# Optimization experiments

Measured on AMD Instinct MI355X. Metric: run time of the kernel, lower is better.

## Reference

```python
import jax, jax.numpy as jnp
import numpy as np

N_NODE = 4095
D_EMB = 32
D_MODEL = 64
NHEADS = 8
ALPHA = 1.0
B = N_NODE + 1  # batch must equal n_node+1 (see einsum 'nm,tmd->tnd')
T = 32


def setup_inputs() -> dict:
    key = jax.random.key(0)
    ks = jax.random.split(key, 16)
    f32 = jnp.float32
    inp = {
        "q": jax.random.normal(ks[0], (B, T, D_MODEL), f32),
        "k": jax.random.normal(ks[1], (B, T, D_MODEL), f32),
        "v": jax.random.normal(ks[2], (B, T, D_MODEL), f32),
        # learned parameters (torch init is randn; scaled for numeric stability)
        "emb": jax.random.normal(ks[3], (N_NODE + 1, D_EMB), f32) * 0.05,
        "We": jax.random.normal(ks[4], (D_EMB, D_MODEL, D_MODEL), f32) * 0.05,
        "be": jax.random.normal(ks[5], (D_EMB, D_MODEL), f32) * 0.05,
        "Wq": jax.random.normal(ks[6], (D_MODEL, D_MODEL), f32) * 0.05,
        "bq": jax.random.normal(ks[7], (D_MODEL,), f32) * 0.05,
        "Wk": jax.random.normal(ks[8], (D_MODEL, D_MODEL), f32) * 0.05,
        "bk": jax.random.normal(ks[9], (D_MODEL,), f32) * 0.05,
        "Wv": jax.random.normal(ks[10], (D_MODEL, D_MODEL), f32) * 0.05,
        "bv": jax.random.normal(ks[11], (D_MODEL,), f32) * 0.05,
        "Wo": jax.random.normal(ks[12], (D_MODEL, D_MODEL), f32) * 0.05,
        "bo": jax.random.normal(ks[13], (D_MODEL,), f32) * 0.05,
    }
    return inp


def _elu(x, alpha):
    return jnp.where(x > 0, x, alpha * (jnp.exp(x) - 1.0))


def _split_heads(x, h):
    # torch.cat(torch.split(x, D//h, dim=-1), dim=0): [B,T,D] -> [h*B,T,D/h]
    b, t, d = x.shape
    return jnp.moveaxis(x.reshape(b, t, h, d // h), 2, 0).reshape(h * b, t, d // h)


def _merge_heads(x, b, h):
    # torch.cat(torch.split(x, B, dim=0), dim=-1): [h*B,T,D/h] -> [B,T,D]
    hb, t, dh = x.shape
    return jnp.moveaxis(x.reshape(h, b, t, dh), 0, 2).reshape(b, t, h * dh)


def reference(q, k, v, emb, We, be, Wq, bq, Wk, bk, Wv, bv, Wo, bo):
    Bq, Tq, D = q.shape
    h = NHEADS
    scale = (D // h) ** 0.5

    # linear projections (torch Linear: x @ W.T + b)
    q = q @ Wq.T + bq
    k = k @ Wk.T + bk
    v = v @ Wv.T + bv

    # adjacency: sum over d_emb of pairwise diff == s_i - s_j (same math, no [N,N,E] tensor)
    s = jnp.sum(emb, axis=-1)  # [N+1]
    sim = s[:, None] - s[None, :]  # [N+1, N+1]
    A = jax.nn.softmax(_elu(sim, ALPHA), axis=-1) + jnp.eye(Bq, dtype=q.dtype)

    # updateQ: adjacency-weighted diffusion + per-node weight matrices
    qt = jnp.transpose(q, (1, 0, 2))  # [T, N, D]
    W = jnp.einsum('ne,eio->nio', emb, We)  # [N, D, D]
    b = emb @ be  # [N, D]
    q_ = jnp.einsum('nm,tmd->tnd', A, qt)  # diffusion
    q_ = jnp.einsum('tnd,ndo->tno', q_, W) + b  # per-node matmul
    q = jnp.transpose(q_, (1, 0, 2))  # [N, T, D]

    # manual multi-head attention via split/cat
    qh = _split_heads(q, h)
    kh = _split_heads(k, h)
    vh = _split_heads(v, h)
    attn = jax.nn.softmax(jnp.einsum('btd,bsd->bts', qh, kh) / scale, axis=-1)
    out = jnp.einsum('bts,bsd->btd', attn, vh)
    out = _merge_heads(out, Bq, h)
    return out @ Wo.T + bo
```

## Files before the change

kernel.cpp:

```cpp
#include <hip/hip_runtime.h>
#include <hip/hip_bf16.h>

constexpr int NN  = 4096;
constexpr int DE  = 32;
constexpr int TD  = 2048;

typedef __attribute__((ext_vector_type(8))) short short8;
typedef __attribute__((ext_vector_type(4))) float f32x4;

#define MFMA16(a, b, c) __builtin_amdgcn_mfma_f32_16x16x32_bf16(a, b, c, 0, 0, 0)

__device__ inline ushort f2b(float x) {
    __hip_bfloat16 h = __float2bfloat16(x);
    union { __hip_bfloat16 h; ushort u; } c; c.h = h;
    return c.u;
}

__device__ inline float b2f(ushort u) {
    union { unsigned u; float f; } c; c.u = ((unsigned)u) << 16;
    return c.f;
}

__device__ inline short8 pack8(float4 a, float4 b) {
    short8 v;
    v[0] = (short)f2b(a.x); v[1] = (short)f2b(a.y); v[2] = (short)f2b(a.z); v[3] = (short)f2b(a.w);
    v[4] = (short)f2b(b.x); v[5] = (short)f2b(b.y); v[6] = (short)f2b(b.z); v[7] = (short)f2b(b.w);
    return v;
}

__device__ inline short8 pack8v(f32x4 a, f32x4 b) {
    short8 v;
    v[0] = (short)f2b(a[0]); v[1] = (short)f2b(a[1]); v[2] = (short)f2b(a[2]); v[3] = (short)f2b(a[3]);
    v[4] = (short)f2b(b[0]); v[5] = (short)f2b(b[1]); v[6] = (short)f2b(b[2]); v[7] = (short)f2b(b[3]);
    return v;
}

__device__ __forceinline__ short8 as_s8(f32x4 v) {
    union { f32x4 f; short8 s; } u; u.f = v; return u.s;
}

template<int OFF>
__device__ __forceinline__ f32x4 gl16(unsigned long long addr) {
    f32x4 d;
    asm volatile("global_load_dwordx4 %0, %1, off offset:%c2"
                 : "=v"(d) : "v"(addr), "n"(OFF) : "memory");
    return d;
}

__global__ __launch_bounds__(256) void k_prep(const float* __restrict__ emb,
                                              const float* __restrict__ We,
                                              const float* __restrict__ be,
                                              const float* __restrict__ Wk,
                                              const float* __restrict__ Wv,
                                              const float* __restrict__ Wo,
                                              float* __restrict__ s_g,
                                              ushort* __restrict__ embbf,
                                              ushort* __restrict__ WeTT,
                                              ushort* __restrict__ Wkbf,
                                              ushort* __restrict__ Wvbf,
                                              ushort* __restrict__ Wobf,
                                              float* __restrict__ bn) {
    int id = blockIdx.x, tid = threadIdx.x;
    if (id < 16) {
        int n = id * 256 + tid;
        const float4* e4 = (const float4*)(emb + n * DE);
        float s = 0.f;
#pragma unroll
        for (int i = 0; i < DE / 4; ++i) { float4 v = e4[i]; s += v.x + v.y + v.z + v.w; }
        s_g[n] = s;
    } else if (id < 144) {
        int g4 = (id - 16) * 256 + tid;
        float4 v = *(const float4*)&emb[(size_t)g4 * 4];
        ushort4 o; o.x = f2b(v.x); o.y = f2b(v.y); o.z = f2b(v.z); o.w = f2b(v.w);
        *(ushort4*)&embbf[(size_t)g4 * 4] = o;
    } else if (id < 656) {
        int gid = (id - 144) * 256 + tid;
        int od = gid >> 5, e = gid & 31;
        int o = od >> 6, d = od & 63;
        WeTT[gid] = f2b(We[(size_t)e * 4096 + d * 64 + o]);
    } else if (id < 704) {
        int id5 = id - 656;
        int which = id5 >> 4, gid = (id5 & 15) * 256 + tid;
        const float* src = which == 0 ? Wk : (which == 1 ? Wv : Wo);
        ushort* dst = which == 0 ? Wkbf : (which == 1 ? Wvbf : Wobf);
        dst[gid] = f2b(src[gid]);
    } else {
        int gid = (id - 704) * 256 + tid;
        int n = gid >> 6, o = gid & 63;
        float acc = 0.f;
#pragma unroll
        for (int e = 0; e < DE; ++e) acc += emb[n * DE + e] * be[e * 64 + o];
        bn[gid] = acc;
    }
}

__global__ __launch_bounds__(256) void k_pr(const float* __restrict__ X,
                                            const float* __restrict__ W,
                                            const float* __restrict__ bias,
                                            ushort* __restrict__ Y,
                                            const float* __restrict__ s_g,
                                            int* __restrict__ perm) {
    __shared__ float ss[NN];
    int id = blockIdx.x, tid = threadIdx.x;
    if (id < 512) {
        int lane = tid & 63, wid = tid >> 6;
        int r0 = id * 256 + wid * 64;
        int l15 = lane & 15, kb = lane >> 4;
        f32x4 acc[4][4] = {};
#pragma unroll
        for (int kk = 0; kk < 2; ++kk) {
            short8 af[4], bf[4];
#pragma unroll
            for (int f = 0; f < 4; ++f) {
                const float* ap = X + (size_t)(r0 + f * 16 + l15) * 64 + kk * 32 + kb * 8;
                af[f] = pack8(*(const float4*)ap, *(const float4*)(ap + 4));
                const float* bp = W + (size_t)(f * 16 + l15) * 64 + kk * 32 + kb * 8;
                bf[f] = pack8(*(const float4*)bp, *(const float4*)(bp + 4));
            }
#pragma unroll
            for (int i = 0; i < 4; ++i)
#pragma unroll
                for (int j = 0; j < 4; ++j)
                    acc[i][j] = MFMA16(af[i], bf[j], acc[i][j]);
        }
        float bcol[4];
#pragma unroll
        for (int j = 0; j < 4; ++j) bcol[j] = bias[j * 16 + l15];
#pragma unroll
        for (int i = 0; i < 4; ++i)
#pragma unroll
            for (int j = 0; j < 4; ++j)
#pragma unroll
                for (int r = 0; r < 4; ++r)
                    Y[(size_t)(r0 + i * 16 + kb * 4 + r) * 64 + j * 16 + l15] =
                        f2b(acc[i][j][r] + bcol[j]);
    } else {
        for (int i = tid; i < NN; i += 256) ss[i] = s_g[i];
        __syncthreads();
        int g = tid >> 5, l = tid & 31;
        int n = (id - 512) * 8 + g;
        float sn = ss[n];
        int cnt = 0;
        for (int j2 = 0; j2 < 128; ++j2) {
            int m = j2 * 32 + l;
            float sm = ss[m];
            cnt += (sm < sn) || (sm == sn && m < n);
        }
        for (int off = 16; off; off >>= 1) cnt += __shfl_down(cnt, off, 32);
        if (l == 0) perm[cnt] = n;
    }
}

__global__ __launch_bounds__(256) void k_csum(const ushort* __restrict__ qp,
                                              const float* __restrict__ s_g,
                                              const int* __restrict__ perm,
                                              float* __restrict__ Cj,
                                              float* __restrict__ Cb) {
    __shared__ int ns[64];
    __shared__ float bs[64];
    int bx = blockIdx.x, by = blockIdx.y, tid = threadIdx.x;
    if (tid < 64) {
        int n = perm[bx * 64 + tid];
        ns[tid] = n;
        bs[tid] = __expf(-s_g[n]);
    }
    __syncthreads();
    int j = by * 256 + tid;
    float run[8] = {};
    for (int ii = 0; ii < 64; ++ii) {
        float qv = b2f(qp[(size_t)ns[ii] * 2048 + j]);
        float b = bs[ii], t = qv;
#pragma unroll
        for (int k2 = 0; k2 < 8; ++k2) { run[k2] += t; t *= b; }
    }
    float* cp = Cj + ((size_t)bx * 2048 + j) * 8;
    *(float4*)cp       = make_float4(run[0], run[1], run[2], run[3]);
    *(float4*)(cp + 4) = make_float4(run[4], run[5], run[6], run[7]);
    if (by == 0 && tid < 64) {
        float b = bs[tid], bk = 1.f;
#pragma unroll
        for (int k2 = 0; k2 < 8; ++k2) {
            float v = bk;
            for (int off = 32; off; off >>= 1) v += __shfl_down(v, off, 64);
            if (tid == 0) Cb[bx * 8 + k2] = v;
            bk *= b;
        }
    }
}

__global__ __launch_bounds__(256) void k_pre(const float* __restrict__ Cj,
                                             float* __restrict__ PRE) {
    int gid = blockIdx.x * 256 + threadIdx.x;
    float run = 0.f;
    for (int c = 0; c < 64; ++c) {
        PRE[(size_t)c * 16384 + gid] = run;
        run += Cj[(size_t)c * 16384 + gid];
    }
    PRE[(size_t)64 * 16384 + gid] = run;
}

__global__ __launch_bounds__(256) void k_combw(const ushort* __restrict__ qp,
                                               const float* __restrict__ s_g,
                                               const int* __restrict__ perm,
                                               const float* __restrict__ PRE,
                                               const float* __restrict__ Cb,
                                               ushort* __restrict__ qdifb,
                                               const ushort* __restrict__ embbf,
                                               const ushort* __restrict__ WeTT,
                                               ushort* __restrict__ WnT) {
    __shared__ int ns[64];
    __shared__ float sa[64], sb[64];
    int id = blockIdx.x, tid = threadIdx.x;
    if (id < 512) {
        int bx = id & 63, by = id >> 6;
        if (tid < 64) {
            int n = perm[bx * 64 + tid];
            ns[tid] = n;
            float s = s_g[n];
            sa[tid] = __expf(s);
            sb[tid] = __expf(-s);
        }
        __syncthreads();
        int j = by * 256 + tid;
        float T[8], pre[8];
        {
            const float* pp = PRE + (size_t)bx * 16384 + (size_t)j * 8;
            float4 u0 = *(const float4*)pp, u1 = *(const float4*)(pp + 4);
            pre[0] = u0.x; pre[1] = u0.y; pre[2] = u0.z; pre[3] = u0.w;
            pre[4] = u1.x; pre[5] = u1.y; pre[6] = u1.z; pre[7] = u1.w;
            const float* tp = PRE + (size_t)64 * 16384 + (size_t)j * 8;
            float4 t0 = *(const float4*)tp, t1 = *(const float4*)(tp + 4);
            T[0] = t0.x; T[1] = t0.y; T[2] = t0.z; T[3] = t0.w;
            T[4] = t1.x; T[5] = t1.y; T[6] = t1.z; T[7] = t1.w;
        }
        float TB[8] = {}, preb[8] = {};
        for (int c = 0; c < 64; ++c) {
            float4 v0 = *(const float4*)&Cb[c * 8], v1 = *(const float4*)&Cb[c * 8 + 4];
            TB[0] += v0.x; TB[1] += v0.y; TB[2] += v0.z; TB[3] += v0.w;
            TB[4] += v1.x; TB[5] += v1.y; TB[6] += v1.z; TB[7] += v1.w;
            if (c < bx) {
                preb[0] += v0.x; preb[1] += v0.y; preb[2] += v0.z; preb[3] += v0.w;
                preb[4] += v1.x; preb[5] += v1.y; preb[6] += v1.z; preb[7] += v1.w;
            }
        }
        for (int ii = 0; ii < 64; ++ii) {
            int n = ns[ii];
            float a = sa[ii], b = sb[ii];
            float g0 = 0.36787944117144233f;
            float g1 = g0 * a;
            float g2 = g1 * a * 0.5f;
            float g3 = g2 * a * (1.f / 3.f);
            float g4 = g3 * a * 0.25f;
            float g5 = g4 * a * 0.2f;
            float g6 = g5 * a * (1.f / 6.f);
            float g7 = g6 * a * (1.f / 7.f);
            float Z = a * preb[1]
                    + g0 * (TB[0] - preb[0]) + g1 * (TB[1] - preb[1])
                    + g2 * (TB[2] - preb[2]) + g3 * (TB[3] - preb[3])
                    + g4 * (TB[4] - preb[4]) + g5 * (TB[5] - preb[5])
                    + g6 * (TB[6] - preb[6]) + g7 * (TB[7] - preb[7]);
            float izv = 1.f / Z;
            float qv = b2f(qp[(size_t)n * 2048 + j]);
            float ss2 = g0 * (T[0] - pre[0]) + g1 * (T[1] - pre[1])
                      + g2 * (T[2] - pre[2]) + g3 * (T[3] - pre[3])
                      + g4 * (T[4] - pre[4]) + g5 * (T[5] - pre[5])
                      + g6 * (T[6] - pre[6]) + g7 * (T[7] - pre[7]);
            float outv = (a * pre[1] + ss2) * izv + qv;
            qdifb[(size_t)n * 2048 + j] = f2b(outv);
            float bk = 1.f;
#pragma unroll
            for (int k2 = 0; k2 < 8; ++k2) { pre[k2] += bk * qv; preb[k2] += bk; bk *= b; }
        }
    } else {
        int w2 = id - 512;
        int lane = tid & 63, wid = tid >> 6;
        int n0  = (w2 & 31) * 128 + (wid >> 1) * 64;
        int od0 = (w2 >> 5) * 128 + (wid & 1) * 64;
        int l15 = lane & 15, kb = lane >> 4;
        short8 af[4], bf[4];
#pragma unroll
        for (int f = 0; f < 4; ++f) {
            af[f] = *(const short8*)(embbf + (size_t)(n0 + f * 16 + l15) * 32 + kb * 8);
            bf[f] = *(const short8*)(WeTT + (size_t)(od0 + f * 16 + l15) * 32 + kb * 8);
        }
        f32x4 acc[4][4] = {};
#pragma unroll
        for (int i = 0; i < 4; ++i)
#pragma unroll
            for (int j = 0; j < 4; ++j)
                acc[i][j] = MFMA16(af[i], bf[j], acc[i][j]);
#pragma unroll
        for (int i = 0; i < 4; ++i)
#pragma unroll
            for (int j = 0; j < 4; ++j)
#pragma unroll
                for (int r = 0; r < 4; ++r)
                    WnT[(size_t)(n0 + i * 16 + kb * 4 + r) * 4096 + od0 + j * 16 + l15] =
                        f2b(acc[i][j][r]);
    }
}

__global__ __launch_bounds__(128, 2) void k_fused(const float* __restrict__ kin,
                                                  const float* __restrict__ vin,
                                                  const ushort* __restrict__ qdifb,
                                                  const ushort* __restrict__ WnT,
                                                  const float* __restrict__ bn,
                                                  const ushort* __restrict__ Wkbf,
                                                  const float* __restrict__ bk,
                                                  const ushort* __restrict__ Wvbf,
                                                  const float* __restrict__ bv,
                                                  const ushort* __restrict__ Wobf,
                                                  const float* __restrict__ bo,
                                                  float* __restrict__ out) {
    __shared__ ushort Kb[2][512];
    __shared__ ushort Qb[2][512];
    __shared__ ushort Vb[2][512];
    __shared__ ushort attb[2][32 * 72];
    int tid = threadIdx.x, lane = tid & 63, w = tid >> 6;
    int b = blockIdx.x * 2 + w;
    int l15 = lane & 15, g = lane >> 4;

    unsigned long long ka = (unsigned long long)(kin   + (size_t)b * TD   + (8 + l15) * 64 + g * 8);
    unsigned long long va = (unsigned long long)(vin   + (size_t)b * TD   + (8 + l15) * 64 + g * 8);
    unsigned long long qa = (unsigned long long)(qdifb + (size_t)b * TD   + (8 + l15) * 64 + g * 8);
    unsigned long long wa = (unsigned long long)(WnT   + (size_t)b * 4096 + (24 + l15) * 64 + g * 8);
    f32x4 k00a = gl16<-2048>(ka), k00b = gl16<-2032>(ka);
    f32x4 k01a = gl16<-1920>(ka), k01b = gl16<-1904>(ka);
    f32x4 k10a = gl16< 2048>(ka), k10b = gl16< 2064>(ka);
    f32x4 k11a = gl16< 2176>(ka), k11b = gl16< 2192>(ka);
    f32x4 v00a = gl16<-2048>(va), v00b = gl16<-2032>(va);
    f32x4 v01a = gl16<-1920>(va), v01b = gl16<-1904>(va);
    f32x4 v10a = gl16< 2048>(va), v10b = gl16< 2064>(va);
    f32x4 v11a = gl16< 2176>(va), v11b = gl16< 2192>(va);
    f32x4 q00 = gl16<-1024>(qa), q01 = gl16<-960>(qa);
    f32x4 q10 = gl16< 1024>(qa), q11 = gl16<1088>(qa);
    f32x4 w00 = gl16<-3072>(wa), w01 = gl16<-3008>(wa);
    f32x4 w10 = gl16<-1024>(wa), w11 = gl16< -960>(wa);
    f32x4 w20 = gl16< 1024>(wa), w21 = gl16< 1088>(wa);
    f32x4 w30 = gl16< 3072>(wa), w31 = gl16< 3136>(wa);

    float bkc[4], bvc[4], bnc[4], boc[4];
#pragma unroll
    for (int j = 0; j < 4; ++j) {
        bkc[j] = bk[j * 16 + l15];
        bvc[j] = bv[j * 16 + l15];
        bnc[j] = bn[b * 64 + j * 16 + l15];
        boc[j] = bo[j * 16 + l15];
    }

    asm volatile("s_waitcnt vmcnt(0)" ::: "memory");
    __builtin_amdgcn_sched_barrier(0);

    short8 kaf[2][2], vaf[2][2], qaf[2][2], bqf[4][2];
    kaf[0][0] = pack8v(k00a, k00b); kaf[1][0] = pack8v(k01a, k01b);
    kaf[0][1] = pack8v(k10a, k10b); kaf[1][1] = pack8v(k11a, k11b);
    vaf[0][0] = pack8v(v00a, v00b); vaf[1][0] = pack8v(v01a, v01b);
    vaf[0][1] = pack8v(v10a, v10b); vaf[1][1] = pack8v(v11a, v11b);
    qaf[0][0] = as_s8(q00); qaf[1][0] = as_s8(q01);
    qaf[0][1] = as_s8(q10); qaf[1][1] = as_s8(q11);
    bqf[0][0] = as_s8(w00); bqf[0][1] = as_s8(w01);
    bqf[1][0] = as_s8(w10); bqf[1][1] = as_s8(w11);
    bqf[2][0] = as_s8(w20); bqf[2][1] = as_s8(w21);
    bqf[3][0] = as_s8(w30); bqf[3][1] = as_s8(w31);

    const float SCALE = 0.35355339059327373f;
    short8 zfrag = {};
    int hh_w = l15 >> 3, d1_w = l15 & 7;

#pragma unroll
    for (int j = 0; j < 4; ++j) {
        f32x4 ak[2] = {}, aq[2] = {}, av[2] = {};
#pragma unroll
        for (int kk = 0; kk < 2; ++kk) {
            short8 bkfj = *(const short8*)(Wkbf + (size_t)(j * 16 + l15) * 64 + kk * 32 + g * 8);
            short8 bvfj = *(const short8*)(Wvbf + (size_t)(j * 16 + l15) * 64 + kk * 32 + g * 8);
#pragma unroll
            for (int ti = 0; ti < 2; ++ti) {
                ak[ti] = MFMA16(kaf[kk][ti], bkfj, ak[ti]);
                aq[ti] = MFMA16(qaf[kk][ti], bqf[j][kk], aq[ti]);
                av[ti] = MFMA16(vaf[kk][ti], bvfj, av[ti]);
            }
        }
#pragma unroll
        for (int ti = 0; ti < 2; ++ti) {
#pragma unroll
            for (int r = 0; r < 4; ++r) {
                int s = ti * 16 + g * 4 + r;
                Kb[w][hh_w * 256 + s * 8 + d1_w] = f2b(ak[ti][r] + bkc[j]);
                Qb[w][hh_w * 256 + s * 8 + d1_w] = f2b(aq[ti][r] + bnc[j]);
            }
#pragma unroll
            for (int r = 0; r < 4; r += 2) {
                int s = ti * 16 + g * 4 + r;
                ushort2 p; p.x = f2b(av[ti][r] + bvc[j]); p.y = f2b(av[ti][r + 1] + bvc[j]);
                *(ushort2*)&Vb[w][hh_w * 256 + d1_w * 32 + s] = p;
            }
        }
#pragma unroll
        for (int hh = 0; hh < 2; ++hh) {
            int h = j * 2 + hh;
            short8 kf[2], qf[2];
#pragma unroll
            for (int si = 0; si < 2; ++si)
                kf[si] = (lane < 16) ? *(const short8*)&Kb[w][hh * 256 + (si * 16 + l15) * 8] : zfrag;
#pragma unroll
            for (int ti = 0; ti < 2; ++ti)
                qf[ti] = (lane < 16) ? *(const short8*)&Qb[w][hh * 256 + (ti * 16 + l15) * 8] : zfrag;
            f32x4 sc[2][2];
#pragma unroll
            for (int si = 0; si < 2; ++si)
#pragma unroll
                for (int ti = 0; ti < 2; ++ti)
                    sc[si][ti] = MFMA16(kf[si], qf[ti], f32x4{});
            unsigned pq[2][2][2];
#pragma unroll
            for (int ti = 0; ti < 2; ++ti) {
                float e0[4], e1[4], sm = 0.f;
#pragma unroll
                for (int r = 0; r < 4; ++r) {
                    e0[r] = __expf(sc[0][ti][r] * SCALE);
                    e1[r] = __expf(sc[1][ti][r] * SCALE);
                    sm += e0[r] + e1[r];
                }
                sm += __shfl_xor(sm, 16);
                sm += __shfl_xor(sm, 32);
                float inv = 1.f / sm;
                pq[0][ti][0] = (unsigned)f2b(e0[0] * inv) | ((unsigned)f2b(e0[1] * inv) << 16);
                pq[0][ti][1] = (unsigned)f2b(e0[2] * inv) | ((unsigned)f2b(e0[3] * inv) << 16);
                pq[1][ti][0] = (unsigned)f2b(e1[0] * inv) | ((unsigned)f2b(e1[1] * inv) << 16);
                pq[1][ti][1] = (unsigned)f2b(e1[2] * inv) | ((unsigned)f2b(e1[3] * inv) << 16);
            }
            short8 vf = *(const short8*)&Vb[w][hh * 256 + (l15 & 7) * 32 + g * 8];
            int L0 = l15 + ((g & 1) << 5);
            int L1 = L0 + 16;
            bool s1 = (g >> 1) != 0;
#pragma unroll
            for (int ti = 0; ti < 2; ++ti) {
                unsigned a00 = __shfl(pq[0][ti][0], L0), a01 = __shfl(pq[0][ti][1], L0);
                unsigned a10 = __shfl(pq[1][ti][0], L0), a11 = __shfl(pq[1][ti][1], L0);
                unsigned b00 = __shfl(pq[0][ti][0], L1), b01 = __shfl(pq[0][ti][1], L1);
                unsigned b10 = __shfl(pq[1][ti][0], L1), b11 = __shfl(pq[1][ti][1], L1);
                union { unsigned uu[4]; short8 s8; } af;
                af.uu[0] = s1 ? a10 : a00; af.uu[1] = s1 ? a11 : a01;
                af.uu[2] = s1 ? b10 : b00; af.uu[3] = s1 ? b11 : b01;
                f32x4 pv = MFMA16(af.s8, vf, f32x4{});
                if (l15 < 8) {
#pragma unroll
                    for (int r = 0; r < 4; ++r)
                        attb[w][(ti * 16 + g * 4 + r) * 72 + h * 8 + l15] = f2b(pv[r]);
                }
            }
        }
    }

    short8 aof[2][2];
#pragma unroll
    for (int kk = 0; kk < 2; ++kk)
#pragma unroll
        for (int ti = 0; ti < 2; ++ti)
            aof[kk][ti] = *(const short8*)&attb[w][(ti * 16 + l15) * 72 + kk * 32 + g * 8];
    f32x4 co[2][4] = {};
#pragma unroll
    for (int kk = 0; kk < 2; ++kk)
#pragma unroll
        for (int j = 0; j < 4; ++j) {
            short8 bf = *(const short8*)(Wobf + (size_t)(j * 16 + l15) * 64 + kk * 32 + g * 8);
#pragma unroll
            for (int ti = 0; ti < 2; ++ti)
                co[ti][j] = MFMA16(aof[kk][ti], bf, co[ti][j]);
        }
#pragma unroll
    for (int ti = 0; ti < 2; ++ti)
#pragma unroll
        for (int j = 0; j < 4; ++j)
#pragma unroll
            for (int r = 0; r < 4; ++r)
                out[(size_t)b * TD + (ti * 16 + g * 4 + r) * 64 + j * 16 + l15] =
                    co[ti][j][r] + boc[j];
}

extern "C" void kernel_launch(void* const* d_in, const int* in_sizes, int n_in,
                              void* d_out, int out_size, void* d_ws, size_t ws_size,
                              hipStream_t stream) {
    const float* q   = (const float*)d_in[0];
    const float* k   = (const float*)d_in[1];
    const float* v   = (const float*)d_in[2];
    const float* emb = (const float*)d_in[3];
    const float* We  = (const float*)d_in[4];
    const float* be  = (const float*)d_in[5];
    const float* Wq  = (const float*)d_in[6];
    const float* bq  = (const float*)d_in[7];
    const float* Wk  = (const float*)d_in[8];
    const float* bk  = (const float*)d_in[9];
    const float* Wv  = (const float*)d_in[10];
    const float* bv  = (const float*)d_in[11];
    const float* Wo  = (const float*)d_in[12];
    const float* bo  = (const float*)d_in[13];

    float* ws = (float*)d_ws;
    ushort* qp    = (ushort*)ws;
    ushort* WnT   = (ushort*)(ws + 4194304);
    ushort* qdifb = (ushort*)(ws + 12582912);
    float*  Cj    = ws + 16777216;
    float*  bn    = ws + 17825792;
    float*  s_g   = ws + 18087936;
    int*    perm  = (int*)(ws + 18092032);
    float*  Cb    = ws + 18096128;
    ushort* embbf = (ushort*)(ws + 18096640);
    ushort* WeTT  = (ushort*)(ws + 18162176);
    ushort* Wkbf  = (ushort*)(ws + 18227712);
    ushort* Wvbf  = (ushort*)(ws + 18229760);
    ushort* Wobf  = (ushort*)(ws + 18231808);
    float*  PRE   = ws + 18233856;
    float*  outp  = (float*)d_out;

    k_prep <<<1728, 256, 0, stream>>>(emb, We, be, Wk, Wv, Wo,
                                      s_g, embbf, WeTT, Wkbf, Wvbf, Wobf, bn);
    k_pr   <<<1024, 256, 0, stream>>>(q, Wq, bq, qp, s_g, perm);
    k_csum <<<dim3(64, 8), 256, 0, stream>>>(qp, s_g, perm, Cj, Cb);
    k_pre  <<<64, 256, 0, stream>>>(Cj, PRE);
    k_combw<<<1536, 256, 0, stream>>>(qp, s_g, perm, PRE, Cb, qdifb,
                                      embbf, WeTT, WnT);
    k_fused<<<2048, 128, 0, stream>>>(k, v, qdifb, WnT, bn,
                                      Wkbf, bk, Wvbf, bv, Wobf, bo, outp);
}
```

Measured before the change: 123.2 us.

## Precompute Cb prefix sums, pad LDS tiles, route softmax probs through LDS

Adds an extra block to k_pre that computes prefix sums of Cb once, so each k_combw thread no longer loops over 64 Cb entries with a conditional accumulate. In k_fused, the K/Q/V shared tiles get padded strides to reduce LDS bank conflicts. The softmax probabilities are written to a new padded LDS buffer and read back as MFMA A-fragments, replacing the cross-lane shuffle/select sequence. This uses more LDS per block and adds a small serial scan on one block.

```diff
diff --git a/kernel.cpp b/kernel.cpp
--- a/kernel.cpp
+++ b/kernel.cpp
@@ -189,21 +189,39 @@
 }
 
 __global__ __launch_bounds__(256) void k_pre(const float* __restrict__ Cj,
-                                             float* __restrict__ PRE) {
-    int gid = blockIdx.x * 256 + threadIdx.x;
-    float run = 0.f;
-    for (int c = 0; c < 64; ++c) {
-        PRE[(size_t)c * 16384 + gid] = run;
-        run += Cj[(size_t)c * 16384 + gid];
-    }
-    PRE[(size_t)64 * 16384 + gid] = run;
+                                             float* __restrict__ PRE,
+                                             const float* __restrict__ Cb,
+                                             float* __restrict__ CbPre) {
+    __shared__ float sCb[512];
+    int tid = threadIdx.x;
+    if (blockIdx.x < 64) {
+        int gid = blockIdx.x * 256 + tid;
+        float run = 0.f;
+        for (int c = 0; c < 64; ++c) {
+            PRE[(size_t)c * 16384 + gid] = run;
+            run += Cj[(size_t)c * 16384 + gid];
+        }
+        PRE[(size_t)64 * 16384 + gid] = run;
+    } else {
+        sCb[tid] = Cb[tid];
+        sCb[tid + 256] = Cb[tid + 256];
+        __syncthreads();
+        if (tid < 8) {
+            float run = 0.f;
+            for (int c = 0; c < 64; ++c) {
+                CbPre[c * 8 + tid] = run;
+                run += sCb[c * 8 + tid];
+            }
+            CbPre[512 + tid] = run;
+        }
+    }
 }
 
 __global__ __launch_bounds__(256) void k_combw(const ushort* __restrict__ qp,
                                                const float* __restrict__ s_g,
                                                const int* __restrict__ perm,
                                                const float* __restrict__ PRE,
-                                               const float* __restrict__ Cb,
+                                               const float* __restrict__ CbPre,
                                                ushort* __restrict__ qdifb,
                                                const ushort* __restrict__ embbf,
                                                const ushort* __restrict__ WeTT,
@@ -233,15 +251,14 @@
             T[0] = t0.x; T[1] = t0.y; T[2] = t0.z; T[3] = t0.w;
             T[4] = t1.x; T[5] = t1.y; T[6] = t1.z; T[7] = t1.w;
         }
-        float TB[8] = {}, preb[8] = {};
-        for (int c = 0; c < 64; ++c) {
-            float4 v0 = *(const float4*)&Cb[c * 8], v1 = *(const float4*)&Cb[c * 8 + 4];
-            TB[0] += v0.x; TB[1] += v0.y; TB[2] += v0.z; TB[3] += v0.w;
-            TB[4] += v1.x; TB[5] += v1.y; TB[6] += v1.z; TB[7] += v1.w;
-            if (c < bx) {
-                preb[0] += v0.x; preb[1] += v0.y; preb[2] += v0.z; preb[3] += v0.w;
-                preb[4] += v1.x; preb[5] += v1.y; preb[6] += v1.z; preb[7] += v1.w;
-            }
+        float TB[8], preb[8];
+        {
+            float4 v0 = *(const float4*)&CbPre[bx * 8], v1 = *(const float4*)&CbPre[bx * 8 + 4];
+            preb[0] = v0.x; preb[1] = v0.y; preb[2] = v0.z; preb[3] = v0.w;
+            preb[4] = v1.x; preb[5] = v1.y; preb[6] = v1.z; preb[7] = v1.w;
+            float4 t0 = *(const float4*)&CbPre[512], t1 = *(const float4*)&CbPre[516];
+            TB[0] = t0.x; TB[1] = t0.y; TB[2] = t0.z; TB[3] = t0.w;
+            TB[4] = t1.x; TB[5] = t1.y; TB[6] = t1.z; TB[7] = t1.w;
         }
         for (int ii = 0; ii < 64; ++ii) {
             int n = ns[ii];
@@ -312,9 +329,10 @@
                                                   const ushort* __restrict__ Wobf,
                                                   const float* __restrict__ bo,
                                                   float* __restrict__ out) {
-    __shared__ ushort Kb[2][512];
-    __shared__ ushort Qb[2][512];
-    __shared__ ushort Vb[2][512];
+    __shared__ ushort Kb[2][544];
+    __shared__ ushort Qb[2][544];
+    __shared__ ushort Vb[2][640];
+    __shared__ ushort Pb[2][1280];
     __shared__ ushort attb[2][32 * 72];
     int tid = threadIdx.x, lane = tid & 63, w = tid >> 6;
     int b = blockIdx.x * 2 + w;
@@ -386,14 +404,14 @@
 #pragma unroll
             for (int r = 0; r < 4; ++r) {
                 int s = ti * 16 + g * 4 + r;
-                Kb[w][hh_w * 256 + s * 8 + d1_w] = f2b(ak[ti][r] + bkc[j]);
-                Qb[w][hh_w * 256 + s * 8 + d1_w] = f2b(aq[ti][r] + bnc[j]);
+                Kb[w][hh_w * 272 + s * 8 + d1_w] = f2b(ak[ti][r] + bkc[j]);
+                Qb[w][hh_w * 272 + s * 8 + d1_w] = f2b(aq[ti][r] + bnc[j]);
             }
 #pragma unroll
             for (int r = 0; r < 4; r += 2) {
                 int s = ti * 16 + g * 4 + r;
                 ushort2 p; p.x = f2b(av[ti][r] + bvc[j]); p.y = f2b(av[ti][r + 1] + bvc[j]);
-                *(ushort2*)&Vb[w][hh_w * 256 + d1_w * 32 + s] = p;
+                *(ushort2*)&Vb[w][hh_w * 320 + d1_w * 40 + s] = p;
             }
         }
 #pragma unroll
@@ -402,17 +420,16 @@
             short8 kf[2], qf[2];
 #pragma unroll
             for (int si = 0; si < 2; ++si)
-                kf[si] = (lane < 16) ? *(const short8*)&Kb[w][hh * 256 + (si * 16 + l15) * 8] : zfrag;
+                kf[si] = (lane < 16) ? *(const short8*)&Kb[w][hh * 272 + (si * 16 + l15) * 8] : zfrag;
 #pragma unroll
             for (int ti = 0; ti < 2; ++ti)
-                qf[ti] = (lane < 16) ? *(const short8*)&Qb[w][hh * 256 + (ti * 16 + l15) * 8] : zfrag;
+                qf[ti] = (lane < 16) ? *(const short8*)&Qb[w][hh * 272 + (ti * 16 + l15) * 8] : zfrag;
             f32x4 sc[2][2];
 #pragma unroll
             for (int si = 0; si < 2; ++si)
 #pragma unroll
                 for (int ti = 0; ti < 2; ++ti)
                     sc[si][ti] = MFMA16(kf[si], qf[ti], f32x4{});
-            unsigned pq[2][2][2];
 #pragma unroll
             for (int ti = 0; ti < 2; ++ti) {
                 float e0[4], e1[4], sm = 0.f;
@@ -425,25 +442,21 @@
                 sm += __shfl_xor(sm, 16);
                 sm += __shfl_xor(sm, 32);
                 float inv = 1.f / sm;
-                pq[0][ti][0] = (unsigned)f2b(e0[0] * inv) | ((unsigned)f2b(e0[1] * inv) << 16);
-                pq[0][ti][1] = (unsigned)f2b(e0[2] * inv) | ((unsigned)f2b(e0[3] * inv) << 16);
-                pq[1][ti][0] = (unsigned)f2b(e1[0] * inv) | ((unsigned)f2b(e1[1] * inv) << 16);
-                pq[1][ti][1] = (unsigned)f2b(e1[2] * inv) | ((unsigned)f2b(e1[3] * inv) << 16);
-            }
-            short8 vf = *(const short8*)&Vb[w][hh * 256 + (l15 & 7) * 32 + g * 8];
-            int L0 = l15 + ((g & 1) << 5);
-            int L1 = L0 + 16;
-            bool s1 = (g >> 1) != 0;
+                int t = ti * 16 + l15;
+                unsigned p00 = (unsigned)f2b(e0[0] * inv) | ((unsigned)f2b(e0[1] * inv) << 16);
+                unsigned p01 = (unsigned)f2b(e0[2] * inv) | ((unsigned)f2b(e0[3] * inv) << 16);
+                unsigned p10 = (unsigned)f2b(e1[0] * inv) | ((unsigned)f2b(e1[1] * inv) << 16);
+                unsigned p11 = (unsigned)f2b(e1[2] * inv) | ((unsigned)f2b(e1[3] * inv) << 16);
+                *(unsigned*)&Pb[w][t * 40 + g * 4]          = p00;
+                *(unsigned*)&Pb[w][t * 40 + g * 4 + 2]      = p01;
+                *(unsigned*)&Pb[w][t * 40 + 16 + g * 4]     = p10;
+                *(unsigned*)&Pb[w][t * 40 + 16 + g * 4 + 2] = p11;
+            }
+            short8 vf = *(const short8*)&Vb[w][hh * 320 + (l15 & 7) * 40 + g * 8];
 #pragma unroll
             for (int ti = 0; ti < 2; ++ti) {
-                unsigned a00 = __shfl(pq[0][ti][0], L0), a01 = __shfl(pq[0][ti][1], L0);
-                unsigned a10 = __shfl(pq[1][ti][0], L0), a11 = __shfl(pq[1][ti][1], L0);
-                unsigned b00 = __shfl(pq[0][ti][0], L1), b01 = __shfl(pq[0][ti][1], L1);
-                unsigned b10 = __shfl(pq[1][ti][0], L1), b11 = __shfl(pq[1][ti][1], L1);
-                union { unsigned uu[4]; short8 s8; } af;
-                af.uu[0] = s1 ? a10 : a00; af.uu[1] = s1 ? a11 : a01;
-                af.uu[2] = s1 ? b10 : b00; af.uu[3] = s1 ? b11 : b01;
-                f32x4 pv = MFMA16(af.s8, vf, f32x4{});
+                short8 af = *(const short8*)&Pb[w][(ti * 16 + l15) * 40 + g * 8];
+                f32x4 pv = MFMA16(af, vf, f32x4{});
                 if (l15 < 8) {
 #pragma unroll
                     for (int r = 0; r < 4; ++r)
@@ -512,14 +525,15 @@
     ushort* Wvbf  = (ushort*)(ws + 18229760);
     ushort* Wobf  = (ushort*)(ws + 18231808);
     float*  PRE   = ws + 18233856;
+    float*  CbPre = ws + 19298816;
     float*  outp  = (float*)d_out;
 
     k_prep <<<1728, 256, 0, stream>>>(emb, We, be, Wk, Wv, Wo,
                                       s_g, embbf, WeTT, Wkbf, Wvbf, Wobf, bn);
     k_pr   <<<1024, 256, 0, stream>>>(q, Wq, bq, qp, s_g, perm);
     k_csum <<<dim3(64, 8), 256, 0, stream>>>(qp, s_g, perm, Cj, Cb);
-    k_pre  <<<64, 256, 0, stream>>>(Cj, PRE);
-    k_combw<<<1536, 256, 0, stream>>>(qp, s_g, perm, PRE, Cb, qdifb,
+    k_pre  <<<65, 256, 0, stream>>>(Cj, PRE, Cb, CbPre);
+    k_combw<<<1536, 256, 0, stream>>>(qp, s_g, perm, PRE, CbPre, qdifb,
                                       embbf, WeTT, WnT);
     k_fused<<<2048, 128, 0, stream>>>(k, v, qdifb, WnT, bn,
                                       Wkbf, bk, Wvbf, bv, Wobf, bo, outp);
```

Result: faster. 116.1 us (-5.7%).
